# Optimization experiments

Measured on AMD Instinct MI355X. Metric: run time of the kernel, lower is better.

The kernel has to match this reference:

```python
import jax, jax.numpy as jnp
import numpy as np


def setup_inputs() -> dict:
    key = jax.random.key(0)
    N, H, CH, T = 4, 8, 64, 2048
    qkv = jax.random.normal(key, (N, 3 * H * CH, T), dtype=jnp.float32)
    return {"qkv": qkv, "n_heads": H}


def reference(qkv, n_heads):
    bs, width, length = qkv.shape
    ch = width // (3 * n_heads)
    q, k, v = jnp.split(qkv, 3, axis=1)  # each [bs, H*ch, T]
    q = q.reshape(bs * n_heads, ch, length)
    k = k.reshape(bs * n_heads, ch, length)
    v = v.reshape(bs * n_heads, ch, length)
    scale = 1.0 / jnp.sqrt(jnp.sqrt(jnp.asarray(ch, dtype=qkv.dtype)))
    # [bs*H, T, T] score matrix (non-flash, materialized as in the original)
    weight = jnp.einsum('bct,bcs->bts', q * scale, k * scale)
    weight = jax.nn.softmax(weight.astype(jnp.float32), axis=-1).astype(qkv.dtype)
    a = jnp.einsum('bts,bcs->bct', weight, v)  # [bs*H, ch, T]
    return a.reshape(bs, n_heads * ch, length)
```

## Files before the change

kernel.cpp:

```cpp
#include <hip/hip_runtime.h>


typedef __bf16 bf8v __attribute__((ext_vector_type(8)));
typedef float f4 __attribute__((ext_vector_type(4)));
typedef int i4 __attribute__((ext_vector_type(4)));

#define SEQ 2048
#define DD 64
#define NHEADS 32
#define QBLK 128
#define SBLK 64
#define NTILES (SEQ / SBLK)
#define TILEK (SBLK * DD)
#define STR 68
#define NTHR 256

#define KSC 0.35355339059327373f
#define QSC (0.35355339059327373f * 1.4426950408889634f)

#if __has_builtin(__builtin_amdgcn_exp2f)
#define EXP2(x) __builtin_amdgcn_exp2f(x)
#else
#define EXP2(x) exp2f(x)
#endif

__device__ __forceinline__ void gload16(i4& dst, const __bf16* p) {
    asm volatile("global_load_dwordx4 %0, %1, off" : "=&v"(dst) : "v"(p));
}

#define VMWAIT0() do { asm volatile("s_waitcnt vmcnt(0)" ::: "memory"); \
                       __builtin_amdgcn_sched_barrier(0); } while (0)
#define SBAR() __builtin_amdgcn_sched_barrier(0)

__global__ void prep_kernel(const float* __restrict__ qkv,
                            __bf16* __restrict__ KT, __bf16* __restrict__ Vb) {
    const int bx = blockIdx.x, tid = threadIdx.x;
    if (bx < 256) {
        const int head = bx >> 3, sblk = bx & 7;
        const int b = head >> 3, h = head & 7;
        const float* kp = qkv + (size_t)(b * 1536 + 512 + h * 64) * SEQ;
        __bf16* dst = KT + (size_t)head * SEQ * DD;
        const int s = sblk * 256 + tid;
#pragma unroll
        for (int c0 = 0; c0 < DD; c0 += 8) {
            bf8v v;
#pragma unroll
            for (int j = 0; j < 8; ++j)
                v[j] = (__bf16)(kp[(size_t)(c0 + j) * SEQ + s] * KSC);
            *(bf8v*)(dst + (size_t)s * DD + c0) = v;
        }
    } else {
        const int job = bx - 256;
        const int head = job >> 4, part = job & 15;
        const int b = head >> 3, h = head & 7;
        const float* vp = qkv + (size_t)(b * 1536 + 1024 + h * 64) * SEQ;
        __bf16* dst = Vb + (size_t)head * DD * SEQ;
#pragma unroll
        for (int i = 0; i < 4; ++i) {
            const int e = part * 8192 + (i * 256 + tid) * 8;
            const float4* f = (const float4*)(vp + e);
            float4 a = f[0], c = f[1];
            bf8v o;
            o[0] = (__bf16)a.x; o[1] = (__bf16)a.y; o[2] = (__bf16)a.z; o[3] = (__bf16)a.w;
            o[4] = (__bf16)c.x; o[5] = (__bf16)c.y; o[6] = (__bf16)c.z; o[7] = (__bf16)c.w;
            *(bf8v*)(dst + e) = o;
        }
    }
}

__device__ __forceinline__ bf8v ldswz(const __bf16* base, int r, int c16) {
    return *(const bf8v*)(base + r * DD + (((c16) ^ (r & 7)) << 3));
}

__global__ __launch_bounds__(NTHR, 2) void attn_kernel(
    const float* __restrict__ qkv, const __bf16* __restrict__ KT,
    const __bf16* __restrict__ Vb, float* __restrict__ out)
{
    __shared__ __bf16 KL[2][TILEK];
    __shared__ __bf16 VL[2][TILEK];
    __shared__ __bf16 Ps[QBLK * STR];

    const int tid = threadIdx.x;
    const int wid = tid >> 6;
    const int lane = tid & 63;
    const int g = lane >> 4;
    const int l15 = lane & 15;

    const int bid = blockIdx.x;
    const int bx = (bid & 7) * 64 + (bid >> 3);
    const int head = bx >> 4;
    const int t0 = (bx & 15) * QBLK;
    const int b = head >> 3, h = head & 7;

    const float* qp = qkv + (size_t)(b * 1536 + h * 64) * SEQ;
    const __bf16* kt = KT + (size_t)head * SEQ * DD;
    const __bf16* vb = Vb + (size_t)head * DD * SEQ;
    float* op = out + (size_t)head * DD * SEQ;

    const int sp  = tid & 7;
    const int sr  = tid >> 3;
    const int scs = sp ^ (sr & 7);
    const __bf16* kg0 = kt + sr * DD + (scs << 3);
    const __bf16* kg1 = kt + (sr + 32) * DD + (scs << 3);
    const __bf16* vg0 = vb + (size_t)sr * SEQ + (scs << 3);
    const __bf16* vg1 = vb + (size_t)(sr + 32) * SEQ + (scs << 3);
    const int l0 = sr * DD + (sp << 3);
    const int l1 = (sr + 32) * DD + (sp << 3);

    i4 rk0, rk1, rv0, rv1;

    SBAR();
    gload16(rk0, kg0);
    gload16(rk1, kg1);
    gload16(rv0, vg0);
    gload16(rv1, vg1);
    SBAR();

    bf8v qf[2][2];
    {
        const int tq = t0 + wid * 32 + l15;
#pragma unroll
        for (int ts = 0; ts < 2; ++ts)
#pragma unroll
            for (int ks = 0; ks < 2; ++ks) {
                bf8v q;
#pragma unroll
                for (int j = 0; j < 8; ++j)
                    q[j] = (__bf16)(qp[(size_t)(ks * 32 + g * 8 + j) * SEQ + tq + ts * 16] * QSC);
                qf[ts][ks] = q;
            }
    }

    f4 Oacc[4][2];
#pragma unroll
    for (int ms = 0; ms < 4; ++ms) {
        Oacc[ms][0] = (f4){0.f, 0.f, 0.f, 0.f};
        Oacc[ms][1] = (f4){0.f, 0.f, 0.f, 0.f};
    }
    float lper[2] = {0.f, 0.f};

    VMWAIT0();
    *(i4*)&KL[0][l0] = rk0;  *(i4*)&KL[0][l1] = rk1;
    *(i4*)&VL[0][l0] = rv0;  *(i4*)&VL[0][l1] = rv1;
    __syncthreads();

    for (int it = 0; it < NTILES; ++it) {
        const int cb = it & 1;
        const __bf16* kcu = KL[cb];
        const __bf16* vcu = VL[cb];
        const bool more = (it + 1 < NTILES);

        if (more) {
            const int nx = it + 1;
            SBAR();
            gload16(rk0, kg0 + nx * TILEK);
            gload16(rk1, kg1 + nx * TILEK);
            gload16(rv0, vg0 + nx * SBLK);
            gload16(rv1, vg1 + nx * SBLK);
            SBAR();
        }

        f4 S[4][2];
#pragma unroll
        for (int ss = 0; ss < 4; ++ss) {
            S[ss][0] = (f4){0.f, 0.f, 0.f, 0.f};
            S[ss][1] = (f4){0.f, 0.f, 0.f, 0.f};
        }
        __builtin_amdgcn_s_setprio(1);
#pragma unroll
        for (int ks = 0; ks < 2; ++ks)
#pragma unroll
            for (int ss = 0; ss < 4; ++ss) {
                bf8v a = ldswz(kcu, ss * 16 + l15, ks * 4 + g);
                S[ss][0] = __builtin_amdgcn_mfma_f32_16x16x32_bf16(a, qf[0][ks], S[ss][0], 0, 0, 0);
                S[ss][1] = __builtin_amdgcn_mfma_f32_16x16x32_bf16(a, qf[1][ks], S[ss][1], 0, 0, 0);
            }
        __builtin_amdgcn_s_setprio(0);

        bf8v vf[4][2];
#pragma unroll
        for (int ms = 0; ms < 4; ++ms)
#pragma unroll
            for (int ks = 0; ks < 2; ++ks)
                vf[ms][ks] = ldswz(vcu, ms * 16 + l15, ks * 4 + g);

#pragma unroll
        for (int ts = 0; ts < 2; ++ts) {
            float p[4][4];
            float tsum = 0.f;
#pragma unroll
            for (int ss = 0; ss < 4; ++ss)
#pragma unroll
                for (int r = 0; r < 4; ++r) {
                    float e = EXP2(S[ss][ts][r]);
                    p[ss][r] = e;
                    tsum += e;
                }
            lper[ts] += tsum;

            const int trow = wid * 32 + ts * 16 + l15;
#pragma unroll
            for (int ss = 0; ss < 4; ++ss) {
                union { __bf16 h[4]; uint2 u; } pk;
                pk.h[0] = (__bf16)p[ss][0]; pk.h[1] = (__bf16)p[ss][1];
                pk.h[2] = (__bf16)p[ss][2]; pk.h[3] = (__bf16)p[ss][3];
                *(uint2*)(Ps + trow * STR + ss * 16 + g * 4) = pk.u;
            }
        }

        bf8v pf0[2], pf1[2];
#pragma unroll
        for (int ks = 0; ks < 2; ++ks) {
            union { uint2 u[2]; bf8v b; } u0, u1;
            u0.u[0] = *(const uint2*)(Ps + (wid * 32 + l15) * STR + ks * 32 + g * 8);
            u0.u[1] = *(const uint2*)(Ps + (wid * 32 + l15) * STR + ks * 32 + g * 8 + 4);
            u1.u[0] = *(const uint2*)(Ps + (wid * 32 + 16 + l15) * STR + ks * 32 + g * 8);
            u1.u[1] = *(const uint2*)(Ps + (wid * 32 + 16 + l15) * STR + ks * 32 + g * 8 + 4);
            pf0[ks] = u0.b;
            pf1[ks] = u1.b;
        }

        if (more) {
            VMWAIT0();
            __bf16* kn = (__bf16*)KL[cb ^ 1];
            __bf16* vn = (__bf16*)VL[cb ^ 1];
            *(i4*)&kn[l0] = rk0;  *(i4*)&kn[l1] = rk1;
            *(i4*)&vn[l0] = rv0;  *(i4*)&vn[l1] = rv1;
            __syncthreads();
        }

        __builtin_amdgcn_s_setprio(1);
#pragma unroll
        for (int ks = 0; ks < 2; ++ks)
#pragma unroll
            for (int ms = 0; ms < 4; ++ms) {
                Oacc[ms][0] = __builtin_amdgcn_mfma_f32_16x16x32_bf16(vf[ms][ks], pf0[ks], Oacc[ms][0], 0, 0, 0);
                Oacc[ms][1] = __builtin_amdgcn_mfma_f32_16x16x32_bf16(vf[ms][ks], pf1[ks], Oacc[ms][1], 0, 0, 0);
            }
        __builtin_amdgcn_s_setprio(0);
    }

#pragma unroll
    for (int ts = 0; ts < 2; ++ts) {
        float l = lper[ts];
        l += __shfl_xor(l, 16);
        l += __shfl_xor(l, 32);
        const float rl = 1.0f / l;
        const int t = t0 + wid * 32 + ts * 16 + l15;
#pragma unroll
        for (int ms = 0; ms < 4; ++ms)
#pragma unroll
            for (int r = 0; r < 4; ++r)
                op[(size_t)(ms * 16 + g * 4 + r) * SEQ + t] = Oacc[ms][ts][r] * rl;
    }
}

extern "C" void kernel_launch(void* const* d_in, const int* in_sizes, int n_in,
                              void* d_out, int out_size, void* d_ws, size_t ws_size,
                              hipStream_t stream) {
    const float* qkv = (const float*)d_in[0];
    float* out = (float*)d_out;
    __bf16* KT = (__bf16*)d_ws;
    __bf16* Vb = KT + (size_t)NHEADS * SEQ * DD;
    prep_kernel<<<dim3(256 + 512), dim3(NTHR), 0, stream>>>(qkv, KT, Vb);
    attn_kernel<<<dim3(NHEADS * (SEQ / QBLK)), dim3(NTHR), 0, stream>>>(qkv, KT, Vb, out);
}
```

Measured before the change: 62.17 us.

## Feed P to PV MFMA directly from registers via 16x16x16 bf16 MFMA

The softmax probabilities no longer go through a shared-memory staging buffer. The S accumulator layout is reused directly as the B operand of the 16x16x16 bf16 MFMA, with V fragments loaded as 4-element pieces to match. This removes the LDS write/read round trip and its shared memory footprint. In exchange it uses twice as many MFMA instructions of half the K depth, each with a lower peak rate than 16x16x32, plus more, smaller LDS loads for V.

```diff
diff --git a/kernel.cpp b/kernel.cpp
--- a/kernel.cpp
+++ b/kernel.cpp
@@ -2,6 +2,8 @@
 
 
 typedef __bf16 bf8v __attribute__((ext_vector_type(8)));
+typedef __bf16 bf4 __attribute__((ext_vector_type(4)));
+typedef short s4 __attribute__((ext_vector_type(4)));
 typedef float f4 __attribute__((ext_vector_type(4)));
 typedef int i4 __attribute__((ext_vector_type(4)));
 
@@ -12,7 +14,6 @@
 #define SBLK 64
 #define NTILES (SEQ / SBLK)
 #define TILEK (SBLK * DD)
-#define STR 68
 #define NTHR 256
 
 #define KSC 0.35355339059327373f
@@ -31,6 +32,20 @@
 #define VMWAIT0() do { asm volatile("s_waitcnt vmcnt(0)" ::: "memory"); \
                        __builtin_amdgcn_sched_barrier(0); } while (0)
 #define SBAR() __builtin_amdgcn_sched_barrier(0)
+
+#if __has_builtin(__builtin_amdgcn_mfma_f32_16x16x16bf16_1k)
+__device__ __forceinline__ f4 mfma16(bf4 a, bf4 b, f4 c) {
+    union U { bf4 v; s4 s; };
+    U ua; ua.v = a;
+    U ub; ub.v = b;
+    return __builtin_amdgcn_mfma_f32_16x16x16bf16_1k(ua.s, ub.s, c, 0, 0, 0);
+}
+#else
+__device__ __forceinline__ f4 mfma16(bf4 a, bf4 b, f4 c) {
+    asm("v_mfma_f32_16x16x16_bf16 %0, %1, %2, %0" : "+v"(c) : "v"(a), "v"(b));
+    return c;
+}
+#endif
 
 __global__ void prep_kernel(const float* __restrict__ qkv,
                             __bf16* __restrict__ KT, __bf16* __restrict__ Vb) {
@@ -71,6 +86,10 @@
 __device__ __forceinline__ bf8v ldswz(const __bf16* base, int r, int c16) {
     return *(const bf8v*)(base + r * DD + (((c16) ^ (r & 7)) << 3));
 }
+__device__ __forceinline__ bf4 ldswz4(const __bf16* base, int r, int sloc) {
+    const int c16 = sloc >> 3, off = sloc & 7;
+    return *(const bf4*)(base + r * DD + (((c16) ^ (r & 7)) << 3) + off);
+}
 
 __global__ __launch_bounds__(NTHR, 2) void attn_kernel(
     const float* __restrict__ qkv, const __bf16* __restrict__ KT,
@@ -78,7 +97,6 @@
 {
     __shared__ __bf16 KL[2][TILEK];
     __shared__ __bf16 VL[2][TILEK];
-    __shared__ __bf16 Ps[QBLK * STR];
 
     const int tid = threadIdx.x;
     const int wid = tid >> 6;
@@ -177,47 +195,29 @@
             }
         __builtin_amdgcn_s_setprio(0);
 
-        bf8v vf[4][2];
+        bf4 vf[4][4];
 #pragma unroll
         for (int ms = 0; ms < 4; ++ms)
 #pragma unroll
-            for (int ks = 0; ks < 2; ++ks)
-                vf[ms][ks] = ldswz(vcu, ms * 16 + l15, ks * 4 + g);
-
+            for (int ss = 0; ss < 4; ++ss)
+                vf[ms][ss] = ldswz4(vcu, ms * 16 + l15, ss * 16 + g * 4);
+
+        bf4 pb[2][4];
 #pragma unroll
         for (int ts = 0; ts < 2; ++ts) {
-            float p[4][4];
             float tsum = 0.f;
 #pragma unroll
-            for (int ss = 0; ss < 4; ++ss)
+            for (int ss = 0; ss < 4; ++ss) {
+                bf4 q;
 #pragma unroll
                 for (int r = 0; r < 4; ++r) {
                     float e = EXP2(S[ss][ts][r]);
-                    p[ss][r] = e;
                     tsum += e;
+                    q[r] = (__bf16)e;
                 }
+                pb[ts][ss] = q;
+            }
             lper[ts] += tsum;
-
-            const int trow = wid * 32 + ts * 16 + l15;
-#pragma unroll
-            for (int ss = 0; ss < 4; ++ss) {
-                union { __bf16 h[4]; uint2 u; } pk;
-                pk.h[0] = (__bf16)p[ss][0]; pk.h[1] = (__bf16)p[ss][1];
-                pk.h[2] = (__bf16)p[ss][2]; pk.h[3] = (__bf16)p[ss][3];
-                *(uint2*)(Ps + trow * STR + ss * 16 + g * 4) = pk.u;
-            }
-        }
-
-        bf8v pf0[2], pf1[2];
-#pragma unroll
-        for (int ks = 0; ks < 2; ++ks) {
-            union { uint2 u[2]; bf8v b; } u0, u1;
-            u0.u[0] = *(const uint2*)(Ps + (wid * 32 + l15) * STR + ks * 32 + g * 8);
-            u0.u[1] = *(const uint2*)(Ps + (wid * 32 + l15) * STR + ks * 32 + g * 8 + 4);
-            u1.u[0] = *(const uint2*)(Ps + (wid * 32 + 16 + l15) * STR + ks * 32 + g * 8);
-            u1.u[1] = *(const uint2*)(Ps + (wid * 32 + 16 + l15) * STR + ks * 32 + g * 8 + 4);
-            pf0[ks] = u0.b;
-            pf1[ks] = u1.b;
         }
 
         if (more) {
@@ -231,14 +231,16 @@
 
         __builtin_amdgcn_s_setprio(1);
 #pragma unroll
-        for (int ks = 0; ks < 2; ++ks)
+        for (int ss = 0; ss < 4; ++ss)
 #pragma unroll
             for (int ms = 0; ms < 4; ++ms) {
-                Oacc[ms][0] = __builtin_amdgcn_mfma_f32_16x16x32_bf16(vf[ms][ks], pf0[ks], Oacc[ms][0], 0, 0, 0);
-                Oacc[ms][1] = __builtin_amdgcn_mfma_f32_16x16x32_bf16(vf[ms][ks], pf1[ks], Oacc[ms][1], 0, 0, 0);
+                Oacc[ms][0] = mfma16(vf[ms][ss], pb[0][ss], Oacc[ms][0]);
+                Oacc[ms][1] = mfma16(vf[ms][ss], pb[1][ss], Oacc[ms][1]);
             }
         __builtin_amdgcn_s_setprio(0);
     }
+
+    asm volatile("s_nop 7\n\ts_nop 7" :::);
 
 #pragma unroll
     for (int ts = 0; ts < 2; ++ts) {
```

Measured after the change: 71.05 us. 1.14x slower.
